# Performance work log

Hardware: AMD Instinct MI355X
Metric: run time of the kernel (lower is better)

The kernel has to match this reference:

```python
import jax, jax.numpy as jnp
import numpy as np

T = 2048          # num_tokens (flattened vLLM format)
HID = 4096        # hidden_size
H = 32            # query heads
HKV = 8           # kv heads (GQA)
G = H // HKV      # queries per kv head
D = HID // H      # head_dim = 128
W = 64            # loop_window_size (sliding window, includes current token)
THETA = 10000.0   # rope base
SCALE = D ** -0.5
NEG = -1e9


def setup_inputs() -> dict:
    key = jax.random.key(0)
    ks = jax.random.split(key, 8)
    return {
        "positions": jnp.arange(T, dtype=jnp.int32),
        "hidden_states": jax.random.normal(ks[0], (T, HID), jnp.float32),
        # loop-0 global KV cache (already RoPE'd keys, as vLLM caches them)
        "k_global": jax.random.normal(ks[1], (T, HKV, D), jnp.float32),
        "v_global": jax.random.normal(ks[2], (T, HKV, D), jnp.float32),
        "w_qkv": jax.random.normal(ks[3], ((H + 2 * HKV) * D, HID), jnp.float32) * (HID ** -0.5),
        "w_o": jax.random.normal(ks[4], (HID, H * D), jnp.float32) * ((H * D) ** -0.5),
        "w_gate": jax.random.normal(ks[5], (H, D), jnp.float32) * (D ** -0.5),
        "b_gate": jnp.zeros((H,), jnp.float32),
    }


def _rope(x, pos):
    # neox-style rotary: x [T, h, D]
    half = D // 2
    inv_freq = 1.0 / (THETA ** (jnp.arange(half, dtype=jnp.float32) / half))
    f = pos.astype(jnp.float32)[:, None] * inv_freq[None, :]   # [T, half]
    cos = jnp.cos(f)[:, None, :]
    sin = jnp.sin(f)[:, None, :]
    x1, x2 = x[..., :half], x[..., half:]
    return jnp.concatenate([x1 * cos - x2 * sin, x2 * cos + x1 * sin], axis=-1)


def reference(positions, hidden_states, k_global, v_global, w_qkv, w_o, w_gate, b_gate):
    # loop_idx > 0 path: global (loop-0 KV) + local sliding-window attention, sigmoid gate blend
    qkv = hidden_states @ w_qkv.T                               # [T, (H+2*HKV)*D]
    q, k, v = jnp.split(qkv, [H * D, H * D + HKV * D], axis=-1)
    q = _rope(q.reshape(T, H, D), positions)                    # [T, H, D]
    k = _rope(k.reshape(T, HKV, D), positions)                  # [T, HKV, D]
    v = v.reshape(T, HKV, D)
    qg = q.reshape(T, HKV, G, D)

    # --- global causal attention against loop-0 cached KV ---
    s = jnp.einsum('tghd,sgd->ghts', qg, k_global) * SCALE      # [HKV, G, T, T]
    causal = positions[:, None] >= positions[None, :]
    s = jnp.where(causal[None, None], s, NEG)
    a = jax.nn.softmax(s, axis=-1)
    out_g = jnp.einsum('ghts,sgd->tghd', a, v_global).reshape(T, H * D)

    # --- local sliding-window causal attention on current KV (banded, no T x T) ---
    t = jnp.arange(T)
    idx = t[:, None] - (W - 1) + jnp.arange(W)[None, :]          # [T, W] keys i-W+1..i
    valid = idx >= 0
    idxc = jnp.clip(idx, 0, T - 1)
    kw = k[idxc]                                                 # [T, W, HKV, D]
    vw = v[idxc]
    sl = jnp.einsum('tghd,twgd->ghtw', qg, kw) * SCALE           # [HKV, G, T, W]
    sl = jnp.where(valid[None, None], sl, NEG)
    al = jax.nn.softmax(sl, axis=-1)
    out_l = jnp.einsum('ghtw,twgd->tghd', al, vw).reshape(T, H * D)

    # --- per-head sigmoid gate (diagonal trick == per-head dot product) ---
    gate = jax.nn.sigmoid(jnp.einsum('thd,hd->th', q, w_gate) + b_gate)  # [T, H]
    gate = jnp.broadcast_to(gate[:, :, None], (T, H, D)).reshape(T, H * D)

    out = out_g * gate + out_l * (1.0 - gate)
    return out @ w_o.T                                           # [T, HID]
```

## Files before the change

kernel.cpp:

```cpp
#include <hip/hip_runtime.h>
#include <hip/hip_bf16.h>
#include <math.h>

#define T 2048
#define HID 4096
#define NH 32
#define NKV 8
#define DH 128
#define QKV_N 6144
#define SCALE_F 0.08838834764831845f
#define NEGV -1e9f

typedef unsigned short u16t;
typedef __attribute__((ext_vector_type(8))) short bf8;
typedef __attribute__((ext_vector_type(4))) float f4;

__device__ __forceinline__ float bf2f(u16t x) {
  unsigned int u = ((unsigned int)x) << 16;
  return __builtin_bit_cast(float, u);
}
__device__ __forceinline__ u16t f2bf(float f) {
  unsigned int u = __builtin_bit_cast(unsigned int, f);
  u += 0x7fffu + ((u >> 16) & 1u);
  return (u16t)(u >> 16);
}

template <int F32>
__device__ __forceinline__ bf8 load8(const void* p, size_t idx) {
  if (F32) {
    const f4* fp = (const f4*)((const float*)p + idx);
    f4 a = fp[0], b = fp[1];
    bf8 r;
    r[0] = (short)f2bf(a[0]); r[1] = (short)f2bf(a[1]);
    r[2] = (short)f2bf(a[2]); r[3] = (short)f2bf(a[3]);
    r[4] = (short)f2bf(b[0]); r[5] = (short)f2bf(b[1]);
    r[6] = (short)f2bf(b[2]); r[7] = (short)f2bf(b[3]);
    return r;
  }
  return *(const bf8*)((const u16t*)p + idx);
}

__device__ __forceinline__ void gl_lds16(const u16t* g, u16t* l) {
  __builtin_amdgcn_global_load_lds(
      (const __attribute__((address_space(1))) void*)g,
      (__attribute__((address_space(3))) void*)l, 16, 0, 0);
}

__global__ __launch_bounds__(256) void cvt_bf16(const float* __restrict__ in,
                                                u16t* __restrict__ out, int n8) {
  int i = blockIdx.x * 256 + threadIdx.x;
  if (i >= n8) return;
  const f4* fp = (const f4*)(in + (size_t)i * 8);
  f4 a = fp[0], b = fp[1];
  bf8 r;
  r[0] = (short)f2bf(a[0]); r[1] = (short)f2bf(a[1]);
  r[2] = (short)f2bf(a[2]); r[3] = (short)f2bf(a[3]);
  r[4] = (short)f2bf(b[0]); r[5] = (short)f2bf(b[1]);
  r[6] = (short)f2bf(b[2]); r[7] = (short)f2bf(b[3]);
  *(bf8*)(out + (size_t)i * 8) = r;
}

template <int OUT32>
__global__ __launch_bounds__(256) void gemm_bt_bf(const u16t* __restrict__ A,
                                                  const u16t* __restrict__ B,
                                                  void* __restrict__ C, int N, int K) {
  __shared__ alignas(16) u16t As[128 * 64];
  __shared__ alignas(16) u16t Bs[128 * 64];
  const int tid = threadIdx.x;
  const int wave = tid >> 6, lane = tid & 63;
  const int l15 = lane & 15, quad = lane >> 4;
  unsigned nwg = gridDim.x * gridDim.y;
  unsigned lin = blockIdx.y * gridDim.x + blockIdx.x;
  lin = (lin & 7) * (nwg >> 3) + (lin >> 3);
  const int bx = lin % gridDim.x, by = lin / gridDim.x;
  const int m0 = by * 128, n0 = bx * 128;
  const int wm = (wave & 1) * 64, wn = (wave >> 1) * 64;

  const int sr = tid >> 3, skc = (tid & 7) << 3;
  const u16t* Ag = A + (size_t)(m0 + sr) * K + skc;
  const u16t* Bg = B + (size_t)(n0 + sr) * K + skc;

  f4 acc[4][4];
#pragma unroll
  for (int i = 0; i < 4; i++)
#pragma unroll
    for (int j = 0; j < 4; j++) acc[i][j] = (f4){0.f, 0.f, 0.f, 0.f};

  for (int k0 = 0; k0 < K; k0 += 64) {
    __syncthreads();
#pragma unroll
    for (int i = 0; i < 4; i++) {
      int c = tid + 256 * i;
      gl_lds16(Ag + (size_t)(32 * i) * K + k0, &As[c * 8]);
      gl_lds16(Bg + (size_t)(32 * i) * K + k0, &Bs[c * 8]);
    }
    __syncthreads();
#pragma unroll
    for (int kq = 0; kq < 2; kq++) {
      bf8 af[4], bfr[4];
#pragma unroll
      for (int mt = 0; mt < 4; mt++)
        af[mt] = *(const bf8*)&As[(wm + mt * 16 + l15) * 64 + kq * 32 + quad * 8];
#pragma unroll
      for (int nt = 0; nt < 4; nt++)
        bfr[nt] = *(const bf8*)&Bs[(wn + nt * 16 + l15) * 64 + kq * 32 + quad * 8];
#pragma unroll
      for (int mt = 0; mt < 4; mt++)
#pragma unroll
        for (int nt = 0; nt < 4; nt++)
          acc[mt][nt] = __builtin_amdgcn_mfma_f32_16x16x32_bf16(af[mt], bfr[nt], acc[mt][nt], 0, 0, 0);
    }
  }
#pragma unroll
  for (int mt = 0; mt < 4; mt++)
#pragma unroll
    for (int nt = 0; nt < 4; nt++)
#pragma unroll
      for (int r = 0; r < 4; r++) {
        int row = m0 + wm + mt * 16 + quad * 4 + r;
        int col = n0 + wn + nt * 16 + l15;
        if (OUT32)
          ((float*)C)[(size_t)row * N + col] = acc[mt][nt][r];
        else
          ((u16t*)C)[(size_t)row * N + col] = f2bf(acc[mt][nt][r]);
      }
}

__global__ __launch_bounds__(256) void prep_kernel(
    const int* __restrict__ positions, const u16t* __restrict__ qkv,
    const float* __restrict__ kg_in, const float* __restrict__ wg,
    const float* __restrict__ bg, u16t* __restrict__ Qr, u16t* __restrict__ Kl,
    u16t* __restrict__ KG, float* __restrict__ gate) {
  const int t = blockIdx.x, tid = threadIdx.x;
  const float pos = (float)positions[t];
  const u16t* row = qkv + (size_t)t * QKV_N;
  float gp = 0.f;
#pragma unroll
  for (int i = 0; i < 8; i++) {
    int p = tid * 8 + i;
    int h = p >> 6, dp = p & 63;
    float invf = exp2f(-0.20762050593045702f * (float)dp);
    float f = pos * invf;
    float c = cosf(f), s = sinf(f);
    float x1 = bf2f(row[h * DH + dp]);
    float x2 = bf2f(row[h * DH + dp + 64]);
    float o1 = x1 * c - x2 * s;
    float o2 = x2 * c + x1 * s;
    Qr[(size_t)t * HID + h * DH + dp] = f2bf(o1);
    Qr[(size_t)t * HID + h * DH + dp + 64] = f2bf(o2);
    gp += o1 * wg[h * DH + dp] + o2 * wg[h * DH + dp + 64];
  }
  gp += __shfl_xor(gp, 1, 64);
  gp += __shfl_xor(gp, 2, 64);
  gp += __shfl_xor(gp, 4, 64);
  if ((tid & 7) == 0) {
    int h = tid >> 3;
    gate[t * NH + h] = 1.f / (1.f + expf(-(gp + bg[h])));
  }
  const u16t* krow = row + HID;
#pragma unroll
  for (int i = 0; i < 2; i++) {
    int p = tid * 2 + i;
    int g = p >> 6, dp = p & 63;
    float invf = exp2f(-0.20762050593045702f * (float)dp);
    float f = pos * invf;
    float c = cosf(f), s = sinf(f);
    float x1 = bf2f(krow[g * DH + dp]);
    float x2 = bf2f(krow[g * DH + dp + 64]);
    Kl[(size_t)g * T * DH + t * DH + dp] = f2bf(x1 * c - x2 * s);
    Kl[(size_t)g * T * DH + t * DH + dp + 64] = f2bf(x2 * c + x1 * s);
  }
  {
    int d4 = tid * 4;
    int g = d4 >> 7, d = d4 & 127;
    const float* src = kg_in + (size_t)t * (NKV * DH) + d4;
    u16t* dst = KG + (size_t)g * T * DH + t * DH + d;
    dst[0] = f2bf(src[0]); dst[1] = f2bf(src[1]);
    dst[2] = f2bf(src[2]); dst[3] = f2bf(src[3]);
  }
}

template <int F32>
__global__ __launch_bounds__(256) void transpose_gd(const void* __restrict__ in,
                                                    u16t* __restrict__ out,
                                                    int istride, int coff) {
  __shared__ u16t tile[64][72];
  const int g = blockIdx.z;
  const int t0 = blockIdx.x * 64, d0 = blockIdx.y * 64;
  u16t* dst = out + (size_t)g * DH * T;
  const int tid = threadIdx.x;
#pragma unroll
  for (int i = 0; i < 2; i++) {
    int c = tid + 256 * i;
    int r = c >> 3, dch = (c & 7) << 3;
    size_t idx = (size_t)coff + g * DH + (size_t)(t0 + r) * istride + d0 + dch;
    *(bf8*)&tile[r][dch] = load8<F32>(in, idx);
  }
  __syncthreads();
#pragma unroll
  for (int i = 0; i < 2; i++) {
    int c = tid + 256 * i;
    int d = c >> 3, tch = (c & 7) << 3;
    bf8 v;
#pragma unroll
    for (int j = 0; j < 8; j++) v[j] = tile[tch + j][d];
    *(bf8*)&dst[(size_t)(d0 + d) * T + t0 + tch] = v;
  }
}

template <int LOCAL>
__global__ __launch_bounds__(256) void attn_kernel(
    const u16t* __restrict__ Qr, const u16t* __restrict__ Kbase,
    const u16t* __restrict__ VTbase, const float* __restrict__ gate,
    const u16t* __restrict__ oL, u16t* __restrict__ outp) {
  __shared__ u16t k_lds[64 * 136];
  __shared__ u16t v_lds[128 * 72];
  __shared__ u16t p_lds[128 * 72];
  const int h = blockIdx.x, qt = blockIdx.y;
  const int g = h >> 2;
  const int tid = threadIdx.x, wave = tid >> 6, lane = tid & 63;
  const int l15 = lane & 15, quad = lane >> 4;
  const int q0 = qt * 128 + wave * 32;
  const u16t* K = Kbase + (size_t)g * T * DH;
  const u16t* VT = VTbase + (size_t)g * T * DH;

  bf8 qf[2][4];
#pragma unroll
  for (int mt = 0; mt < 2; mt++)
#pragma unroll
    for (int kq = 0; kq < 4; kq++)
      qf[mt][kq] = *(const bf8*)&Qr[(size_t)(q0 + mt * 16 + l15) * HID + h * DH + kq * 32 + quad * 8];

  f4 oacc[2][8];
  float m_st[2][4], l_st[2][4];
#pragma unroll
  for (int mt = 0; mt < 2; mt++) {
#pragma unroll
    for (int dt = 0; dt < 8; dt++) oacc[mt][dt] = (f4){0.f, 0.f, 0.f, 0.f};
#pragma unroll
    for (int r = 0; r < 4; r++) { m_st[mt][r] = -__builtin_inff(); l_st[mt][r] = 0.f; }
  }

  const int jend = 2 * qt + 2;
  const int jbeg = LOCAL ? (qt > 0 ? 2 * qt - 1 : 0) : 0;
  for (int j = jbeg; j < jend; j++) {
    const int kv0 = j * 64;
    __syncthreads();
#pragma unroll
    for (int i = 0; i < 4; i++) {
      int c = tid + 256 * i;
      int r = c >> 4, dch = (c & 15) << 3;
      *(bf8*)&k_lds[r * 136 + dch] = *(const bf8*)&K[(size_t)(kv0 + r) * DH + dch];
      int dd = c >> 3, kch = (c & 7) << 3;
      *(bf8*)&v_lds[dd * 72 + kch] = *(const bf8*)&VT[(size_t)dd * T + kv0 + kch];
    }
    __syncthreads();
    f4 s[2][4];
#pragma unroll
    for (int nt = 0; nt < 4; nt++) {
      bf8 kb[4];
#pragma unroll
      for (int kq = 0; kq < 4; kq++)
        kb[kq] = *(const bf8*)&k_lds[(nt * 16 + l15) * 136 + kq * 32 + quad * 8];
#pragma unroll
      for (int mt = 0; mt < 2; mt++) {
        f4 a = (f4){0.f, 0.f, 0.f, 0.f};
#pragma unroll
        for (int kq = 0; kq < 4; kq++)
          a = __builtin_amdgcn_mfma_f32_16x16x32_bf16(qf[mt][kq], kb[kq], a, 0, 0, 0);
        s[mt][nt] = a;
      }
    }
#pragma unroll
    for (int mt = 0; mt < 2; mt++)
#pragma unroll
      for (int nt = 0; nt < 4; nt++)
#pragma unroll
        for (int r = 0; r < 4; r++) {
          float v = s[mt][nt][r] * SCALE_F;
          int qq = q0 + mt * 16 + quad * 4 + r;
          int kk = kv0 + nt * 16 + l15;
          bool ok = LOCAL ? (kk <= qq && kk >= qq - 63) : (kk <= qq);
          s[mt][nt][r] = ok ? v : NEGV;
        }
    float alpha[2][4], mn[2][4], rs[2][4];
#pragma unroll
    for (int mt = 0; mt < 2; mt++)
#pragma unroll
      for (int r = 0; r < 4; r++) {
        float rm = fmaxf(fmaxf(s[mt][0][r], s[mt][1][r]), fmaxf(s[mt][2][r], s[mt][3][r]));
        rm = fmaxf(rm, __shfl_xor(rm, 1, 64));
        rm = fmaxf(rm, __shfl_xor(rm, 2, 64));
        rm = fmaxf(rm, __shfl_xor(rm, 4, 64));
        rm = fmaxf(rm, __shfl_xor(rm, 8, 64));
        float m2 = fmaxf(m_st[mt][r], rm);
        alpha[mt][r] = __expf(m_st[mt][r] - m2);
        m_st[mt][r] = m2;
        mn[mt][r] = m2;
        rs[mt][r] = 0.f;
      }
#pragma unroll
    for (int mt = 0; mt < 2; mt++)
#pragma unroll
      for (int nt = 0; nt < 4; nt++)
#pragma unroll
        for (int r = 0; r < 4; r++) {
          float p = __expf(s[mt][nt][r] - mn[mt][r]);
          rs[mt][r] += p;
          p_lds[(wave * 32 + mt * 16 + quad * 4 + r) * 72 + nt * 16 + l15] = f2bf(p);
        }
#pragma unroll
    for (int mt = 0; mt < 2; mt++)
#pragma unroll
      for (int r = 0; r < 4; r++) {
        float t0 = rs[mt][r];
        t0 += __shfl_xor(t0, 1, 64);
        t0 += __shfl_xor(t0, 2, 64);
        t0 += __shfl_xor(t0, 4, 64);
        t0 += __shfl_xor(t0, 8, 64);
        l_st[mt][r] = l_st[mt][r] * alpha[mt][r] + t0;
      }
#pragma unroll
    for (int mt = 0; mt < 2; mt++)
#pragma unroll
      for (int dt = 0; dt < 8; dt++) {
        f4 o = oacc[mt][dt];
        o[0] *= alpha[mt][0]; o[1] *= alpha[mt][1];
        o[2] *= alpha[mt][2]; o[3] *= alpha[mt][3];
        oacc[mt][dt] = o;
      }
    __syncthreads();
    bf8 pa[2][2];
#pragma unroll
    for (int mt = 0; mt < 2; mt++)
#pragma unroll
      for (int kq = 0; kq < 2; kq++)
        pa[mt][kq] = *(const bf8*)&p_lds[(wave * 32 + mt * 16 + l15) * 72 + kq * 32 + quad * 8];
#pragma unroll
    for (int dt = 0; dt < 8; dt++) {
      bf8 vb[2];
#pragma unroll
      for (int kq = 0; kq < 2; kq++)
        vb[kq] = *(const bf8*)&v_lds[(dt * 16 + l15) * 72 + kq * 32 + quad * 8];
#pragma unroll
      for (int mt = 0; mt < 2; mt++) {
        oacc[mt][dt] = __builtin_amdgcn_mfma_f32_16x16x32_bf16(pa[mt][0], vb[0], oacc[mt][dt], 0, 0, 0);
        oacc[mt][dt] = __builtin_amdgcn_mfma_f32_16x16x32_bf16(pa[mt][1], vb[1], oacc[mt][dt], 0, 0, 0);
      }
    }
  }
#pragma unroll
  for (int mt = 0; mt < 2; mt++)
#pragma unroll
    for (int r = 0; r < 4; r++) {
      int tq = q0 + mt * 16 + quad * 4 + r;
      float inv_l = 1.f / l_st[mt][r];
      if (LOCAL) {
#pragma unroll
        for (int dt = 0; dt < 8; dt++) {
          int col = dt * 16 + l15;
          outp[(size_t)tq * HID + h * DH + col] = f2bf(oacc[mt][dt][r] * inv_l);
        }
      } else {
        float gt = gate[tq * NH + h];
#pragma unroll
        for (int dt = 0; dt < 8; dt++) {
          int col = dt * 16 + l15;
          float ov = oacc[mt][dt][r] * inv_l;
          float ol = bf2f(oL[(size_t)tq * HID + h * DH + col]);
          outp[(size_t)tq * HID + h * DH + col] = f2bf(ov * gt + ol * (1.f - gt));
        }
      }
    }
}

extern "C" void kernel_launch(void* const* d_in, const int* in_sizes, int n_in,
                              void* d_out, int out_size, void* d_ws, size_t ws_size,
                              hipStream_t stream) {
  (void)in_sizes; (void)n_in; (void)out_size; (void)ws_size;
  const int* positions = (const int*)d_in[0];
  const float* hidden = (const float*)d_in[1];
  const float* k_global = (const float*)d_in[2];
  const void* v_global = d_in[3];
  const float* w_qkv = (const float*)d_in[4];
  const float* w_o = (const float*)d_in[5];
  const float* w_gate = (const float*)d_in[6];
  const float* b_gate = (const float*)d_in[7];
  float* out = (float*)d_out;

  char* ws = (char*)d_ws;
  size_t off = 0;
  u16t* qkv = (u16t*)(ws + off); off += (size_t)T * QKV_N * 2;
  u16t* Qr  = (u16t*)(ws + off); off += (size_t)T * HID * 2;
  u16t* Kl  = (u16t*)(ws + off); off += (size_t)NKV * T * DH * 2;
  u16t* KG  = (u16t*)(ws + off); off += (size_t)NKV * T * DH * 2;
  u16t* VlT = (u16t*)(ws + off); off += (size_t)NKV * T * DH * 2;
  u16t* VGT = (u16t*)(ws + off); off += (size_t)NKV * T * DH * 2;
  float* gateb = (float*)(ws + off); off += (size_t)T * NH * 4;
  u16t* out_l = (u16t*)(ws + off); off += (size_t)T * HID * 2;
  u16t* out_c = (u16t*)(ws + off); off += (size_t)T * HID * 2;
  u16t* hid_bf  = (u16t*)(ws + off);
  u16t* wqkv_bf = (u16t*)(ws + off + (size_t)T * HID * 2);
  u16t* wo_bf   = hid_bf;

  cvt_bf16<<<(T * HID / 8) / 256, 256, 0, stream>>>(hidden, hid_bf, T * HID / 8);
  cvt_bf16<<<(QKV_N * HID / 8) / 256, 256, 0, stream>>>(w_qkv, wqkv_bf, QKV_N * HID / 8);
  gemm_bt_bf<0><<<dim3(QKV_N / 128, T / 128), 256, 0, stream>>>(hid_bf, wqkv_bf, qkv, QKV_N, HID);
  cvt_bf16<<<(HID * HID / 8) / 256, 256, 0, stream>>>(w_o, wo_bf, HID * HID / 8);
  prep_kernel<<<T, 256, 0, stream>>>(positions, qkv, k_global, w_gate, b_gate, Qr, Kl, KG, gateb);
  transpose_gd<0><<<dim3(T / 64, DH / 64, NKV), 256, 0, stream>>>(qkv, VlT, QKV_N, HID + NKV * DH);
  transpose_gd<1><<<dim3(T / 64, DH / 64, NKV), 256, 0, stream>>>(v_global, VGT, NKV * DH, 0);
  attn_kernel<1><<<dim3(NH, T / 128), 256, 0, stream>>>(Qr, Kl, VlT, nullptr, nullptr, out_l);
  attn_kernel<0><<<dim3(NH, T / 128), 256, 0, stream>>>(Qr, KG, VGT, gateb, out_l, out_c);
  gemm_bt_bf<1><<<dim3(HID / 128, T / 128), 256, 0, stream>>>(out_c, wo_bf, out, HID, HID);
}
```

Measured before the change: 751.3 us.

## Replace 128x128 GEMM with double-buffered 256x256 tile, swizzled LDS, 512 threads

Both projection GEMMs now run through a new kernel with 256x256 output tiles, 8 waves and double-buffered LDS. Global-to-LDS loads for the next K step are interleaved with four MFMA quadrants using explicit vmcnt waits, barriers and setprio. An XOR swizzle on LDS chunks is meant to avoid bank conflicts. The aim is to hide load latency and raise MFMA utilisation, at the cost of fewer workgroups (192 and 128 tiles), which may leave some CUs idle on a 256-CU part, plus a 128 KB LDS footprint.

```diff
diff --git a/kernel.cpp b/kernel.cpp
--- a/kernel.cpp
+++ b/kernel.cpp
@@ -45,6 +45,12 @@
       (const __attribute__((address_space(1))) void*)g,
       (__attribute__((address_space(3))) void*)l, 16, 0, 0);
 }
+
+#define BARR() __builtin_amdgcn_s_barrier()
+#define LGKM0() asm volatile("s_waitcnt lgkmcnt(0)" ::: "memory")
+#define VM4() asm volatile("s_waitcnt vmcnt(4)" ::: "memory")
+#define VM2() asm volatile("s_waitcnt vmcnt(2)" ::: "memory")
+#define VM0() asm volatile("s_waitcnt vmcnt(0)" ::: "memory")
 
 __global__ __launch_bounds__(256) void cvt_bf16(const float* __restrict__ in,
                                                 u16t* __restrict__ out, int n8) {
@@ -60,69 +66,135 @@
   *(bf8*)(out + (size_t)i * 8) = r;
 }
 
+
+__device__ __forceinline__ void stage_ht(const u16t* __restrict__ G, int K,
+                                         int k0, u16t* lds, int tid) {
+#pragma unroll
+  for (int i = 0; i < 2; i++) {
+    int c = tid + 512 * i;
+    int r = c >> 3;
+    int sc = (c & 7) ^ (r & 7);
+    gl_lds16(G + (size_t)r * K + k0 + sc * 8, lds + c * 8);
+  }
+}
+
+template <int NF, int RS>
+__device__ __forceinline__ void ld_fr(bf8 (*f)[2], const u16t* buf, int rb, int quad) {
+#pragma unroll
+  for (int i = 0; i < NF; i++)
+#pragma unroll
+    for (int kq = 0; kq < 2; kq++) {
+      int r = rb + i * RS;
+      int ch = (kq * 4 + quad) ^ (r & 7);
+      f[i][kq] = *(const bf8*)&buf[r * 64 + ch * 8];
+    }
+}
+
+template <int QA, int QB>
+__device__ __forceinline__ void mfma_quad(f4 (*acc)[4], const bf8 (*af)[2],
+                                          const bf8 (*bf_)[2]) {
+#pragma unroll
+  for (int m = 0; m < 4; m++)
+#pragma unroll
+    for (int n = 0; n < 2; n++)
+#pragma unroll
+      for (int kq = 0; kq < 2; kq++)
+        acc[QA * 4 + m][QB * 2 + n] = __builtin_amdgcn_mfma_f32_16x16x32_bf16(
+            af[m][kq], bf_[n][kq], acc[QA * 4 + m][QB * 2 + n], 0, 0, 0);
+}
+
 template <int OUT32>
-__global__ __launch_bounds__(256) void gemm_bt_bf(const u16t* __restrict__ A,
+__global__ __launch_bounds__(512, 2) void gemm256(const u16t* __restrict__ A,
                                                   const u16t* __restrict__ B,
                                                   void* __restrict__ C, int N, int K) {
-  __shared__ alignas(16) u16t As[128 * 64];
-  __shared__ alignas(16) u16t Bs[128 * 64];
+  __shared__ alignas(16) u16t As[2][2][128 * 64];
+  __shared__ alignas(16) u16t Bs[2][2][128 * 64];
   const int tid = threadIdx.x;
   const int wave = tid >> 6, lane = tid & 63;
   const int l15 = lane & 15, quad = lane >> 4;
+  const int wm = wave >> 2, wn = wave & 3;
+
   unsigned nwg = gridDim.x * gridDim.y;
   unsigned lin = blockIdx.y * gridDim.x + blockIdx.x;
   lin = (lin & 7) * (nwg >> 3) + (lin >> 3);
   const int bx = lin % gridDim.x, by = lin / gridDim.x;
-  const int m0 = by * 128, n0 = bx * 128;
-  const int wm = (wave & 1) * 64, wn = (wave >> 1) * 64;
-
-  const int sr = tid >> 3, skc = (tid & 7) << 3;
-  const u16t* Ag = A + (size_t)(m0 + sr) * K + skc;
-  const u16t* Bg = B + (size_t)(n0 + sr) * K + skc;
-
-  f4 acc[4][4];
-#pragma unroll
-  for (int i = 0; i < 4; i++)
+  const int m0 = by * 256, n0 = bx * 256;
+
+  const u16t* A0p = A + (size_t)m0 * K;
+  const u16t* A1p = A0p + (size_t)128 * K;
+  const u16t* B0p = B + (size_t)n0 * K;
+  const u16t* B1p = B0p + (size_t)128 * K;
+
+  const int NT = K >> 6;
+
+  stage_ht(A0p, K, 0, &As[0][0][0], tid);
+  stage_ht(B0p, K, 0, &Bs[0][0][0], tid);
+  stage_ht(B1p, K, 0, &Bs[0][1][0], tid);
+  stage_ht(A1p, K, 0, &As[0][1][0], tid);
+
+  f4 acc[8][4];
+#pragma unroll
+  for (int i = 0; i < 8; i++)
 #pragma unroll
     for (int j = 0; j < 4; j++) acc[i][j] = (f4){0.f, 0.f, 0.f, 0.f};
 
-  for (int k0 = 0; k0 < K; k0 += 64) {
-    __syncthreads();
-#pragma unroll
-    for (int i = 0; i < 4; i++) {
-      int c = tid + 256 * i;
-      gl_lds16(Ag + (size_t)(32 * i) * K + k0, &As[c * 8]);
-      gl_lds16(Bg + (size_t)(32 * i) * K + k0, &Bs[c * 8]);
-    }
-    __syncthreads();
-#pragma unroll
-    for (int kq = 0; kq < 2; kq++) {
-      bf8 af[4], bfr[4];
-#pragma unroll
-      for (int mt = 0; mt < 4; mt++)
-        af[mt] = *(const bf8*)&As[(wm + mt * 16 + l15) * 64 + kq * 32 + quad * 8];
-#pragma unroll
-      for (int nt = 0; nt < 4; nt++)
-        bfr[nt] = *(const bf8*)&Bs[(wn + nt * 16 + l15) * 64 + kq * 32 + quad * 8];
-#pragma unroll
-      for (int mt = 0; mt < 4; mt++)
-#pragma unroll
-        for (int nt = 0; nt < 4; nt++)
-          acc[mt][nt] = __builtin_amdgcn_mfma_f32_16x16x32_bf16(af[mt], bfr[nt], acc[mt][nt], 0, 0, 0);
-    }
-  }
-#pragma unroll
-  for (int mt = 0; mt < 4; mt++)
-#pragma unroll
-    for (int nt = 0; nt < 4; nt++)
+  VM4();
+  BARR();
+
+  bf8 af[4][2], b0f[2][2], b1f[2][2];
+  const int ra = wm * 16 + l15;
+  const int rb = wn * 16 + l15;
+
+#pragma unroll 1
+  for (int t = 0; t < NT; ++t) {
+    const int cur = t & 1, nxt = cur ^ 1;
+    const int kn = (t + 1) << 6;
+    const bool st = (t + 1) < NT;
+    ld_fr<4, 32>(af, &As[cur][0][0], ra, quad);
+    ld_fr<2, 64>(b0f, &Bs[cur][0][0], rb, quad);
+    if (st) stage_ht(A0p, K, kn, &As[nxt][0][0], tid);
+    BARR(); LGKM0();
+    __builtin_amdgcn_s_setprio(1);
+    mfma_quad<0, 0>(acc, af, b0f);
+    __builtin_amdgcn_s_setprio(0);
+    if (st) { VM4(); } else { VM2(); }
+    BARR();
+    ld_fr<2, 64>(b1f, &Bs[cur][1][0], rb, quad);
+    if (st) stage_ht(B0p, K, kn, &Bs[nxt][0][0], tid);
+    BARR(); LGKM0();
+    __builtin_amdgcn_s_setprio(1);
+    mfma_quad<0, 1>(acc, af, b1f);
+    __builtin_amdgcn_s_setprio(0);
+    if (st) { VM4(); } else { VM0(); }
+    BARR();
+    ld_fr<4, 32>(af, &As[cur][1][0], ra, quad);
+    if (st) stage_ht(B1p, K, kn, &Bs[nxt][1][0], tid);
+    BARR(); LGKM0();
+    __builtin_amdgcn_s_setprio(1);
+    mfma_quad<1, 1>(acc, af, b1f);
+    __builtin_amdgcn_s_setprio(0);
+    BARR();
+    if (st) stage_ht(A1p, K, kn, &As[nxt][1][0], tid);
+    BARR();
+    __builtin_amdgcn_s_setprio(1);
+    mfma_quad<1, 0>(acc, af, b0f);
+    __builtin_amdgcn_s_setprio(0);
+    if (st) { VM4(); }
+    BARR();
+  }
+
+#pragma unroll
+  for (int fm = 0; fm < 8; fm++)
+#pragma unroll
+    for (int fn = 0; fn < 4; fn++)
 #pragma unroll
       for (int r = 0; r < 4; r++) {
-        int row = m0 + wm + mt * 16 + quad * 4 + r;
-        int col = n0 + wn + nt * 16 + l15;
+        int row = m0 + fm * 32 + wm * 16 + quad * 4 + r;
+        int col = n0 + fn * 64 + wn * 16 + l15;
         if (OUT32)
-          ((float*)C)[(size_t)row * N + col] = acc[mt][nt][r];
+          ((float*)C)[(size_t)row * N + col] = acc[fm][fn][r];
         else
-          ((u16t*)C)[(size_t)row * N + col] = f2bf(acc[mt][nt][r]);
+          ((u16t*)C)[(size_t)row * N + col] = f2bf(acc[fm][fn][r]);
       }
 }
 
@@ -405,12 +477,12 @@
 
   cvt_bf16<<<(T * HID / 8) / 256, 256, 0, stream>>>(hidden, hid_bf, T * HID / 8);
   cvt_bf16<<<(QKV_N * HID / 8) / 256, 256, 0, stream>>>(w_qkv, wqkv_bf, QKV_N * HID / 8);
-  gemm_bt_bf<0><<<dim3(QKV_N / 128, T / 128), 256, 0, stream>>>(hid_bf, wqkv_bf, qkv, QKV_N, HID);
+  gemm256<0><<<dim3(QKV_N / 256, T / 256), 512, 0, stream>>>(hid_bf, wqkv_bf, qkv, QKV_N, HID);
   cvt_bf16<<<(HID * HID / 8) / 256, 256, 0, stream>>>(w_o, wo_bf, HID * HID / 8);
   prep_kernel<<<T, 256, 0, stream>>>(positions, qkv, k_global, w_gate, b_gate, Qr, Kl, KG, gateb);
   transpose_gd<0><<<dim3(T / 64, DH / 64, NKV), 256, 0, stream>>>(qkv, VlT, QKV_N, HID + NKV * DH);
   transpose_gd<1><<<dim3(T / 64, DH / 64, NKV), 256, 0, stream>>>(v_global, VGT, NKV * DH, 0);
   attn_kernel<1><<<dim3(NH, T / 128), 256, 0, stream>>>(Qr, Kl, VlT, nullptr, nullptr, out_l);
   attn_kernel<0><<<dim3(NH, T / 128), 256, 0, stream>>>(Qr, KG, VGT, gateb, out_l, out_c);
-  gemm_bt_bf<1><<<dim3(HID / 128, T / 128), 256, 0, stream>>>(out_c, wo_bf, out, HID, HID);
-}
+  gemm256<1><<<dim3(HID / 256, T / 256), 512, 0, stream>>>(out_c, wo_bf, out, HID, HID);
+}
```

Measured after the change: 706.5 us. -6.0%, faster.
